# Kernel optimization log

Measured on AMD Instinct MI355X. Metric: run time of the kernel, lower is better.

Reference implementation:

```python
import jax, jax.numpy as jnp
import numpy as np

NUM_CLASSES = 30522


def setup_inputs() -> dict:
    key = jax.random.key(0)
    k1, k2 = jax.random.split(key)
    B, S = 1024, 256
    input_ids = jax.random.randint(k1, (B, S), 0, NUM_CLASSES)  # token ids
    weights = jax.random.uniform(k2, (B, S, 1), dtype=jnp.float32)  # per-token weights
    return {"input_ids": input_ids, "weights": weights}


def reference(input_ids, weights):
    # Torch: one_hot(ids, V) * weights -> (B,S,V), max over dim=1 -> (B,V), cast bf16.
    # Equivalent (without the huge (B,S,V) intermediate): scatter-max of the
    # per-token weight into its vocab slot, with a 0 baseline everywhere
    # (non-matching one-hot entries contribute 0 to the max).
    B, S = input_ids.shape
    w = weights[..., 0]  # (B, S)
    base = jnp.zeros((B, NUM_CLASSES), dtype=weights.dtype)
    b_idx = jnp.arange(B)[:, None]  # (B, 1) broadcasts against (B, S) ids
    out = base.at[b_idx, input_ids].max(w)  # (B, V) scatter-max
    return out.astype(jnp.bfloat16)
```

## Files before the change

kernel.cpp:

```cpp
#include <hip/hip_runtime.h>

#define VOCAB 30522
#define SEQ   256

extern "C" __global__ __launch_bounds__(256)
void TargetEncoder_532575944857_kernel(const int* __restrict__ ids,
                                       const float* __restrict__ ws,
                                       unsigned int* __restrict__ out,
                                       int n_tok) {
    const int t = blockIdx.x * blockDim.x + threadIdx.x;
    if (t >= n_tok) return;

    const int   id = ids[t];
    const float w  = ws[t];
    if ((unsigned)id >= (unsigned)VOCAB) return;

    const unsigned u   = __float_as_uint(w);
    const unsigned val = ((u + 0x7FFFu + ((u >> 16) & 1u)) >> 16) << 16;
    if (val == 0u) return;

    const int b = t >> 8;
    atomicMax(out + ((long long)b * VOCAB + id), val);
}

extern "C" void kernel_launch(void* const* d_in, const int* in_sizes, int n_in,
                              void* d_out, int out_size, void* d_ws, size_t ws_size,
                              hipStream_t stream) {
    const int*   ids = (const int*)d_in[0];
    const float* ws  = (const float*)d_in[1];
    const int n_tok  = in_sizes[0];

    (void)hipMemsetAsync(d_out, 0, (size_t)out_size * sizeof(float), stream);

    TargetEncoder_532575944857_kernel<<<(n_tok + 255) / 256, 256, 0, stream>>>(
        ids, ws, (unsigned int*)d_out, n_tok);
}
```

Baseline: 136.6 us.

## Build each row half in shared memory and write output once, dropping memset

New measurement: 131.8 us. 3.5% less time.

```diff
diff --git a/kernel.cpp b/kernel.cpp
--- a/kernel.cpp
+++ b/kernel.cpp
@@ -2,25 +2,46 @@
 
 #define VOCAB 30522
 #define SEQ   256
+#define CHUNK 15264
+
+__device__ __forceinline__ unsigned bf16_bits(float w) {
+    const unsigned u = __float_as_uint(w);
+    return ((u + 0x7FFFu + ((u >> 16) & 1u)) >> 16) << 16;
+}
 
 extern "C" __global__ __launch_bounds__(256)
 void TargetEncoder_532575944857_kernel(const int* __restrict__ ids,
                                        const float* __restrict__ ws,
                                        unsigned int* __restrict__ out,
-                                       int n_tok) {
-    const int t = blockIdx.x * blockDim.x + threadIdx.x;
-    if (t >= n_tok) return;
+                                       int n_rows) {
+    __shared__ unsigned int tab[CHUNK];
 
-    const int   id = ids[t];
-    const float w  = ws[t];
-    if ((unsigned)id >= (unsigned)VOCAB) return;
+    const int blk  = blockIdx.x;
+    const int b    = blk >> 1;
+    const int c    = blk & 1;
+    const int t    = threadIdx.x;
+    const int base = c * CHUNK;
+    const int lim  = c ? (VOCAB - CHUNK) : CHUNK;
 
-    const unsigned u   = __float_as_uint(w);
-    const unsigned val = ((u + 0x7FFFu + ((u >> 16) & 1u)) >> 16) << 16;
-    if (val == 0u) return;
+    if (b >= n_rows) return;
 
-    const int b = t >> 8;
-    atomicMax(out + ((long long)b * VOCAB + id), val);
+    for (int i = t; i < CHUNK; i += 256) tab[i] = 0u;
+    __syncthreads();
+
+    {
+        const int    tok = b * SEQ + t;
+        const int    id  = ids[tok];
+        const unsigned val = bf16_bits(ws[tok]);
+        const int    loc = id - base;
+        if (val != 0u && (unsigned)loc < (unsigned)lim)
+            atomicMax(&tab[loc], val);
+    }
+    __syncthreads();
+
+    uint2*       dst = (uint2*)(out + (long long)b * VOCAB + base);
+    const uint2* src = (const uint2*)tab;
+    const int n2 = lim >> 1;
+    for (int j = t; j < n2; j += 256) dst[j] = src[j];
 }
 
 extern "C" void kernel_launch(void* const* d_in, const int* in_sizes, int n_in,
@@ -29,9 +50,8 @@
     const int*   ids = (const int*)d_in[0];
     const float* ws  = (const float*)d_in[1];
     const int n_tok  = in_sizes[0];
+    const int n_rows = n_tok / SEQ;
 
-    (void)hipMemsetAsync(d_out, 0, (size_t)out_size * sizeof(float), stream);
-
-    TargetEncoder_532575944857_kernel<<<(n_tok + 255) / 256, 256, 0, stream>>>(
-        ids, ws, (unsigned int*)d_out, n_tok);
+    TargetEncoder_532575944857_kernel<<<dim3(n_rows * 2), dim3(256), 0, stream>>>(
+        ids, ws, (unsigned int*)d_out, n_rows);
 }
```
